# Optimization experiments

Hardware: AMD Instinct MI355X
Metric: run time of the kernel (lower is better)

Reference implementation:

```python
import jax, jax.numpy as jnp
import numpy as np

EPS = 1e-08
SURROGATE_SCALE = 10.0  # SuperSpike surrogate slope

@jax.custom_vjp
def spike_fn(v):
    # Heaviside forward, SuperSpike surrogate gradient backward
    return (v > 0).astype(v.dtype)

def _spike_fwd(v):
    return spike_fn(v), v

def _spike_bwd(v, g):
    return (g / (1.0 + SURROGATE_SCALE * jnp.abs(v)) ** 2,)

spike_fn.defvjp(_spike_fwd, _spike_bwd)


def setup_inputs() -> dict:
    key = jax.random.key(0)
    k1, k2, k3, k4 = jax.random.split(key, 4)
    B, C, T = 64, 256, 2048
    x = jax.random.normal(k1, (B, C, T), dtype=jnp.float32)
    conv_weight = jax.random.normal(k2, (C, C, 3), dtype=jnp.float32) * 0.05
    beta = jnp.clip(0.7 + 0.01 * jax.random.normal(k3, (1,), dtype=jnp.float32), 0.0, 1.0)
    b = jnp.clip(1.0 + 0.01 * jax.random.normal(k4, (C,), dtype=jnp.float32), 0.0, None)
    return {"x": x, "conv_weight": conv_weight, "beta": beta, "b": b}


def reference(x, conv_weight, beta, b):
    # x: (B, C, T); LIF recurrence over T with scaled threshold/reset
    norm = (conv_weight ** 2).sum((1, 2))          # (C,)
    inv_norm = 1.0 / (norm + EPS)                   # (C,)
    B, C, T = x.shape
    xt = jnp.transpose(x, (2, 0, 1))                # (T, B, C)

    def step(carry, inp):
        mem, spk = carry
        rst = spk * (b * norm)                      # einsum ab,b,b->ab
        mem = (mem - rst) * beta + inp * (1.0 - beta)
        mthr = mem * inv_norm - b
        spk = spike_fn(mthr)
        return (mem, spk), spk

    init = (jnp.zeros((B, C), x.dtype), jnp.zeros((B, C), x.dtype))
    _, spk_rec = jax.lax.scan(step, init, xt)       # (T, B, C)
    return jnp.transpose(spk_rec, (1, 2, 0))        # (B, C, T), flatten_output=False
```

## Files before the change

kernel.cpp:

```cpp
#include <hip/hip_runtime.h>

#define C_DIM 256
#define T_DIM 2048
#define B_DIM 64
#define NROWS (B_DIM * C_DIM)
#define SEGS 8
#define SEGL (T_DIM / SEGS)
#define WARM 128
#define PW   64
#define NPH  ((WARM + SEGL) / PW)
#define WARM_PH (WARM / PW)
#define SPITCH 68
#define NSTR 64

__device__ __forceinline__ float sqrn(float v) { return __fmul_rn(v, v); }

__global__ __launch_bounds__(64) void norm_kernel(const float* __restrict__ w,
                                                  const float* __restrict__ b,
                                                  float* __restrict__ bn,
                                                  float* __restrict__ ninv) {
    const int c = blockIdx.x;
    const int k = threadIdx.x;
    __shared__ float q[8];
    if (k < 8) {
        const float* a = w + c * 768 + k * 96;
        float r0 = sqrn(a[0]), r1 = sqrn(a[1]), r2 = sqrn(a[2]), r3 = sqrn(a[3]);
        float r4 = sqrn(a[4]), r5 = sqrn(a[5]), r6 = sqrn(a[6]), r7 = sqrn(a[7]);
        #pragma unroll
        for (int i = 8; i < 96; i += 8) {
            r0 = __fadd_rn(r0, sqrn(a[i + 0]));
            r1 = __fadd_rn(r1, sqrn(a[i + 1]));
            r2 = __fadd_rn(r2, sqrn(a[i + 2]));
            r3 = __fadd_rn(r3, sqrn(a[i + 3]));
            r4 = __fadd_rn(r4, sqrn(a[i + 4]));
            r5 = __fadd_rn(r5, sqrn(a[i + 5]));
            r6 = __fadd_rn(r6, sqrn(a[i + 6]));
            r7 = __fadd_rn(r7, sqrn(a[i + 7]));
        }
        q[k] = __fadd_rn(__fadd_rn(__fadd_rn(r0, r1), __fadd_rn(r2, r3)),
                         __fadd_rn(__fadd_rn(r4, r5), __fadd_rn(r6, r7)));
    }
    __syncthreads();
    if (k == 0) {
        float s = __fadd_rn(__fadd_rn(__fadd_rn(q[0], q[1]), __fadd_rn(q[2], q[3])),
                            __fadd_rn(__fadd_rn(q[4], q[5]), __fadd_rn(q[6], q[7])));
        bn[c]   = __fmul_rn(b[c], s);
        ninv[c] = 1.0f / __fadd_rn(s, 1e-8f);
    }
}

__device__ __forceinline__ float step_fast(float xw, float& mem, int& mask,
                                           float bnc, float beta, float nic, float bc) {
    float m0 = __fmul_rn(mem, beta);
    float m1 = __fmul_rn(__fsub_rn(mem, bnc), beta);
    m0 = __fadd_rn(m0, xw);
    m1 = __fadd_rn(m1, xw);
    int mi = (__float_as_int(m1) & mask) | (__float_as_int(m0) & ~mask);
    mem = __int_as_float(mi);
    float p = __fmul_rn(mem, nic);
    float d = __fsub_rn(bc, p);
    mask = __float_as_int(d) >> 31;
    return __int_as_float(mask & 0x3f800000);
}

#define STEP4_NOSTORE(v)                                                   \
    do {                                                                   \
        float xw0 = __fmul_rn((v).x, omb);                                 \
        float xw1 = __fmul_rn((v).y, omb);                                 \
        float xw2 = __fmul_rn((v).z, omb);                                 \
        float xw3 = __fmul_rn((v).w, omb);                                 \
        (void)step_fast(xw0, mem, mask, bnc, beta, nic, bc);               \
        (void)step_fast(xw1, mem, mask, bnc, beta, nic, bc);               \
        (void)step_fast(xw2, mem, mask, bnc, beta, nic, bc);               \
        (void)step_fast(xw3, mem, mask, bnc, beta, nic, bc);               \
    } while (0)

#define STEP4_STORE(v, o)                                                  \
    do {                                                                   \
        float xw0 = __fmul_rn((v).x, omb);                                 \
        float xw1 = __fmul_rn((v).y, omb);                                 \
        float xw2 = __fmul_rn((v).z, omb);                                 \
        float xw3 = __fmul_rn((v).w, omb);                                 \
        (o).x = step_fast(xw0, mem, mask, bnc, beta, nic, bc);             \
        (o).y = step_fast(xw1, mem, mask, bnc, beta, nic, bc);             \
        (o).z = step_fast(xw2, mem, mask, bnc, beta, nic, bc);             \
        (o).w = step_fast(xw3, mem, mask, bnc, beta, nic, bc);             \
    } while (0)

#define WAITCNT_LGKM0  0xC07F

__global__ __launch_bounds__(64) void lif_seg_kernel(const float* __restrict__ x,
                                                     const float* __restrict__ beta_p,
                                                     const float* __restrict__ b,
                                                     const float* __restrict__ bn,
                                                     const float* __restrict__ ninv,
                                                     float* __restrict__ out) {
    __shared__ __align__(16) float lds[NSTR * SPITCH];

    const int lane = threadIdx.x;
    const int seg  = lane & 7;
    const int row  = blockIdx.x * 8 + (lane >> 3);
    const int c    = row & (C_DIM - 1);

    const float beta = beta_p[0];
    const float omb  = __fsub_rn(1.0f, beta);
    const float bnc  = bn[c];
    const float nic  = ninv[c];
    const float bc   = b[c];

    const int fh = lane >> 4;
    const int fj = lane & 15;

    float mem = 0.0f;
    int   mask = 0;

    float* my = &lds[lane * SPITCH];

    #pragma unroll 1
    for (int P = 0; P < NPH; ++P) {
        #pragma unroll
        for (int q = 0; q < 16; ++q) {
            const int s    = 4 * q + fh;
            const int srow = blockIdx.x * 8 + (s >> 3);
            int rel = (s & 7) * SEGL - WARM + P * PW;
            if (rel < 0) rel = 0;
            const float* g = x + (size_t)srow * T_DIM + rel + 4 * fj;
            float4 v = *(const float4*)g;
            *(float4*)(&lds[s * SPITCH + 4 * fj]) = v;
        }
        __builtin_amdgcn_s_waitcnt(WAITCNT_LGKM0);

        if (P < WARM_PH) {
            #pragma unroll
            for (int g = 0; g < PW / 4; ++g) {
                float4 v = *(const float4*)(my + 4 * g);
                STEP4_NOSTORE(v);
            }
            if (P == WARM_PH - 1) {
                if (seg == 0) { mem = 0.0f; mask = 0; }
            }
        } else {
            #pragma unroll
            for (int g = 0; g < PW / 4; ++g) {
                float4 v = *(const float4*)(my + 4 * g);
                float4 o;
                STEP4_STORE(v, o);
                *(float4*)(my + 4 * g) = o;
            }
            __builtin_amdgcn_s_waitcnt(WAITCNT_LGKM0);

            #pragma unroll
            for (int q = 0; q < 16; ++q) {
                const int s    = 4 * q + fh;
                const int srow = blockIdx.x * 8 + (s >> 3);
                const int rel  = (s & 7) * SEGL - WARM + P * PW;
                float4 v = *(const float4*)(&lds[s * SPITCH + 4 * fj]);
                *(float4*)(out + (size_t)srow * T_DIM + rel + 4 * fj) = v;
            }
        }
    }
}

extern "C" void kernel_launch(void* const* d_in, const int* in_sizes, int n_in,
                              void* d_out, int out_size, void* d_ws, size_t ws_size,
                              hipStream_t stream) {
    const float* x    = (const float*)d_in[0];
    const float* w    = (const float*)d_in[1];
    const float* beta = (const float*)d_in[2];
    const float* b    = (const float*)d_in[3];
    float* out  = (float*)d_out;
    float* bn   = (float*)d_ws;
    float* ninv = bn + C_DIM;

    norm_kernel<<<C_DIM, 64, 0, stream>>>(w, b, bn, ninv);
    lif_seg_kernel<<<(NROWS * SEGS) / NSTR, NSTR, 0, stream>>>(x, beta, b, bn, ninv, out);
}
```

Baseline: 252.5 us.

## Register-prefetch next phase's input tiles to overlap global loads with compute

```diff
diff --git a/kernel.cpp b/kernel.cpp
--- a/kernel.cpp
+++ b/kernel.cpp
@@ -89,12 +89,18 @@
 
 #define WAITCNT_LGKM0  0xC07F
 
-__global__ __launch_bounds__(64) void lif_seg_kernel(const float* __restrict__ x,
-                                                     const float* __restrict__ beta_p,
-                                                     const float* __restrict__ b,
-                                                     const float* __restrict__ bn,
-                                                     const float* __restrict__ ninv,
-                                                     float* __restrict__ out) {
+#define PF_LIST(M) \
+    M(0, pf0)  M(1, pf1)  M(2, pf2)  M(3, pf3)  \
+    M(4, pf4)  M(5, pf5)  M(6, pf6)  M(7, pf7)  \
+    M(8, pf8)  M(9, pf9)  M(10, pf10) M(11, pf11) \
+    M(12, pf12) M(13, pf13) M(14, pf14) M(15, pf15)
+
+__global__ __launch_bounds__(64, 2) void lif_seg_kernel(const float* __restrict__ x,
+                                                        const float* __restrict__ beta_p,
+                                                        const float* __restrict__ b,
+                                                        const float* __restrict__ bn,
+                                                        const float* __restrict__ ninv,
+                                                        float* __restrict__ out) {
     __shared__ __align__(16) float lds[NSTR * SPITCH];
 
     const int lane = threadIdx.x;
@@ -116,18 +122,43 @@
 
     float* my = &lds[lane * SPITCH];
 
+    float4 pf0, pf1, pf2, pf3, pf4, pf5, pf6, pf7;
+    float4 pf8, pf9, pf10, pf11, pf12, pf13, pf14, pf15;
+
+#define PF_LOAD0(q, v)                                                        \
+    {                                                                         \
+        const int s_    = 4 * (q) + fh;                                       \
+        const int srow_ = blockIdx.x * 8 + (s_ >> 3);                         \
+        int rel_ = (s_ & 7) * SEGL - WARM;                         \
+        if (rel_ < 0) rel_ = 0;         \
+        v = *(const float4*)(x + (size_t)srow_ * T_DIM + rel_ + 4 * fj);      \
+    }
+    PF_LIST(PF_LOAD0)
+#undef PF_LOAD0
+
     #pragma unroll 1
     for (int P = 0; P < NPH; ++P) {
-        #pragma unroll
-        for (int q = 0; q < 16; ++q) {
-            const int s    = 4 * q + fh;
-            const int srow = blockIdx.x * 8 + (s >> 3);
-            int rel = (s & 7) * SEGL - WARM + P * PW;
-            if (rel < 0) rel = 0;
-            const float* g = x + (size_t)srow * T_DIM + rel + 4 * fj;
-            float4 v = *(const float4*)g;
-            *(float4*)(&lds[s * SPITCH + 4 * fj]) = v;
-        }
+#define PF_COMMIT(q, v)                                                       \
+        {                                                                     \
+            const int s_ = 4 * (q) + fh;                                      \
+            *(float4*)(&lds[s_ * SPITCH + 4 * fj]) = v;                       \
+        }
+        PF_LIST(PF_COMMIT)
+#undef PF_COMMIT
+
+        if (P + 1 < NPH) {
+#define PF_LOADN(q, v)                                                        \
+            {                                                                 \
+                const int s_    = 4 * (q) + fh;                               \
+                const int srow_ = blockIdx.x * 8 + (s_ >> 3);                 \
+                int rel_ = (s_ & 7) * SEGL - WARM + (P + 1) * PW;             \
+                if (rel_ < 0) rel_ = 0;           \
+                v = *(const float4*)(x + (size_t)srow_ * T_DIM + rel_ + 4 * fj); \
+            }
+            PF_LIST(PF_LOADN)
+#undef PF_LOADN
+        }
+        __builtin_amdgcn_sched_barrier(0);
         __builtin_amdgcn_s_waitcnt(WAITCNT_LGKM0);
 
         if (P < WARM_PH) {
```

Result: no change. 250.0 us (-1.0%).

## Double-buffer input via direct global-to-LDS loads with XOR swizzle

Applied to the files above, without the earlier changes.

```diff
diff --git a/kernel.cpp b/kernel.cpp
--- a/kernel.cpp
+++ b/kernel.cpp
@@ -7,11 +7,11 @@
 #define SEGS 8
 #define SEGL (T_DIM / SEGS)
 #define WARM 128
-#define PW   64
+#define PW   32
 #define NPH  ((WARM + SEGL) / PW)
 #define WARM_PH (WARM / PW)
-#define SPITCH 68
 #define NSTR 64
+#define BUF_F (NSTR * PW)
 
 __device__ __forceinline__ float sqrn(float v) { return __fmul_rn(v, v); }
 
@@ -88,19 +88,34 @@
     } while (0)
 
 #define WAITCNT_LGKM0  0xC07F
-
-__global__ __launch_bounds__(64) void lif_seg_kernel(const float* __restrict__ x,
-                                                     const float* __restrict__ beta_p,
-                                                     const float* __restrict__ b,
-                                                     const float* __restrict__ bn,
-                                                     const float* __restrict__ ninv,
-                                                     float* __restrict__ out) {
-    __shared__ __align__(16) float lds[NSTR * SPITCH];
+#define WAITVM8()  asm volatile("s_waitcnt vmcnt(8)" ::: "memory")
+#define WAITVM16() asm volatile("s_waitcnt vmcnt(16)" ::: "memory")
+
+__device__ __forceinline__ void dma16(const float* gp, float* lp) {
+    __builtin_amdgcn_global_load_lds(
+        (const __attribute__((address_space(1))) void*)gp,
+        (__attribute__((address_space(3))) void*)lp,
+        16, 0, 0);
+}
+
+__global__ __launch_bounds__(64)
+void lif_seg_kernel(const float* __restrict__ x,
+                    const float* __restrict__ beta_p,
+                    const float* __restrict__ b,
+                    const float* __restrict__ bn,
+                    const float* __restrict__ ninv,
+                    float* __restrict__ out) {
+    __shared__ __align__(16) float lds[2 * BUF_F];
 
     const int lane = threadIdx.x;
     const int seg  = lane & 7;
     const int row  = blockIdx.x * 8 + (lane >> 3);
     const int c    = row & (C_DIM - 1);
+    const int lk   = lane & 7;
+
+    const int ds  = lane >> 3;
+    const int du  = lane & 7;
+    const int swz = du ^ ds;
 
     const float beta = beta_p[0];
     const float omb  = __fsub_rn(1.0f, beta);
@@ -108,32 +123,45 @@
     const float nic  = ninv[c];
     const float bc   = b[c];
 
-    const int fh = lane >> 4;
-    const int fj = lane & 15;
-
     float mem = 0.0f;
     int   mask = 0;
 
-    float* my = &lds[lane * SPITCH];
+    {
+        int rel = ds * SEGL - WARM;
+        if (rel < 0) rel = 0;
+        const float* g = x + rel + 4 * swz;
+        #pragma unroll
+        for (int q = 0; q < 8; ++q) {
+            const size_t grow = (size_t)(blockIdx.x * 8 + q);
+            dma16(g + grow * T_DIM, lds + q * (8 * PW));
+        }
+    }
 
     #pragma unroll 1
     for (int P = 0; P < NPH; ++P) {
-        #pragma unroll
-        for (int q = 0; q < 16; ++q) {
-            const int s    = 4 * q + fh;
-            const int srow = blockIdx.x * 8 + (s >> 3);
-            int rel = (s & 7) * SEGL - WARM + P * PW;
+        const int cur = P & 1;
+        float* buf = lds + cur * BUF_F;
+
+        if (P + 1 < NPH) {
+            int rel = ds * SEGL - WARM + (P + 1) * PW;
             if (rel < 0) rel = 0;
-            const float* g = x + (size_t)srow * T_DIM + rel + 4 * fj;
-            float4 v = *(const float4*)g;
-            *(float4*)(&lds[s * SPITCH + 4 * fj]) = v;
-        }
-        __builtin_amdgcn_s_waitcnt(WAITCNT_LGKM0);
+            const float* g = x + rel + 4 * swz;
+            float* dst = lds + (cur ^ 1) * BUF_F;
+            #pragma unroll
+            for (int q = 0; q < 8; ++q) {
+                const size_t grow = (size_t)(blockIdx.x * 8 + q);
+                dma16(g + grow * T_DIM, dst + q * (8 * PW));
+            }
+        }
+
+        if (P <= WARM_PH || P == NPH - 1) { WAITVM8(); } else { WAITVM16(); }
+
+        float* my = buf + lane * PW;
 
         if (P < WARM_PH) {
             #pragma unroll
             for (int g = 0; g < PW / 4; ++g) {
-                float4 v = *(const float4*)(my + 4 * g);
+                float4 v = *(const float4*)(my + 4 * (g ^ lk));
                 STEP4_NOSTORE(v);
             }
             if (P == WARM_PH - 1) {
@@ -142,20 +170,19 @@
         } else {
             #pragma unroll
             for (int g = 0; g < PW / 4; ++g) {
-                float4 v = *(const float4*)(my + 4 * g);
+                float4 v = *(const float4*)(my + 4 * (g ^ lk));
                 float4 o;
                 STEP4_STORE(v, o);
-                *(float4*)(my + 4 * g) = o;
+                *(float4*)(my + 4 * (g ^ lk)) = o;
             }
             __builtin_amdgcn_s_waitcnt(WAITCNT_LGKM0);
 
-            #pragma unroll
-            for (int q = 0; q < 16; ++q) {
-                const int s    = 4 * q + fh;
-                const int srow = blockIdx.x * 8 + (s >> 3);
-                const int rel  = (s & 7) * SEGL - WARM + P * PW;
-                float4 v = *(const float4*)(&lds[s * SPITCH + 4 * fj]);
-                *(float4*)(out + (size_t)srow * T_DIM + rel + 4 * fj) = v;
+            const int rel = ds * SEGL - WARM + P * PW;
+            #pragma unroll
+            for (int q = 0; q < 8; ++q) {
+                const size_t grow = (size_t)(blockIdx.x * 8 + q);
+                float4 v = *(const float4*)(buf + (8 * q + ds) * PW + 4 * swz);
+                *(float4*)(out + grow * T_DIM + rel + 4 * du) = v;
             }
         }
     }
```

Result: no change. 255.3 us (+1.1%).

## Stage whole rows into LDS via global_load_lds with 16 segments per row

Applied to the files above, without the earlier changes.

```diff
diff --git a/kernel.cpp b/kernel.cpp
--- a/kernel.cpp
+++ b/kernel.cpp
@@ -4,14 +4,12 @@
 #define T_DIM 2048
 #define B_DIM 64
 #define NROWS (B_DIM * C_DIM)
-#define SEGS 8
+#define RPB  4
+#define SEGS 16
 #define SEGL (T_DIM / SEGS)
 #define WARM 128
-#define PW   64
-#define NPH  ((WARM + SEGL) / PW)
-#define WARM_PH (WARM / PW)
-#define SPITCH 68
-#define NSTR 64
+#define WG   (WARM / 4)
+#define EG   (SEGL / 4)
 
 __device__ __forceinline__ float sqrn(float v) { return __fmul_rn(v, v); }
 
@@ -89,18 +87,27 @@
 
 #define WAITCNT_LGKM0  0xC07F
 
-__global__ __launch_bounds__(64) void lif_seg_kernel(const float* __restrict__ x,
-                                                     const float* __restrict__ beta_p,
-                                                     const float* __restrict__ b,
-                                                     const float* __restrict__ bn,
-                                                     const float* __restrict__ ninv,
-                                                     float* __restrict__ out) {
-    __shared__ __align__(16) float lds[NSTR * SPITCH];
+__device__ __forceinline__ void dma16(const float* gp, float* lp) {
+    __builtin_amdgcn_global_load_lds(
+        (const __attribute__((address_space(1))) void*)gp,
+        (__attribute__((address_space(3))) void*)lp,
+        16, 0, 0);
+}
+
+__global__ __launch_bounds__(64)
+void lif_seg_kernel(const float* __restrict__ x,
+                    const float* __restrict__ beta_p,
+                    const float* __restrict__ b,
+                    const float* __restrict__ bn,
+                    const float* __restrict__ ninv,
+                    float* __restrict__ out) {
+    __shared__ __align__(16) float lds[RPB * T_DIM];
 
     const int lane = threadIdx.x;
-    const int seg  = lane & 7;
-    const int row  = blockIdx.x * 8 + (lane >> 3);
-    const int c    = row & (C_DIM - 1);
+    const int row  = lane >> 4;
+    const int seg  = lane & 15;
+    const size_t grow = (size_t)blockIdx.x * RPB + row;
+    const int c    = (int)(grow & (C_DIM - 1));
 
     const float beta = beta_p[0];
     const float omb  = __fsub_rn(1.0f, beta);
@@ -108,56 +115,57 @@
     const float nic  = ninv[c];
     const float bc   = b[c];
 
-    const int fh = lane >> 4;
-    const int fj = lane & 15;
+    const size_t xbase = (size_t)blockIdx.x * RPB * T_DIM;
 
+    #pragma unroll
+    for (int j = 0; j < 32; ++j) {
+        const int rj = j >> 3, cj = j & 7;
+        const int p  = cj * 64 + lane;
+        const int l  = p ^ ((p >> 5) & 7);
+        dma16(x + xbase + (size_t)rj * T_DIM + 4 * l,
+              lds + rj * T_DIM + cj * 256);
+    }
+    asm volatile("s_waitcnt vmcnt(0)" ::: "memory");
+
+    float* rbase = lds + row * T_DIM;
     float mem = 0.0f;
     int   mask = 0;
 
-    float* my = &lds[lane * SPITCH];
+    {
+        const int wl0  = (seg - 1) * 32;
+        const int wkey = (seg - 1) & 7;
+        const float* wp = rbase + 4 * (wl0 < 0 ? 0 : wl0);
+        const int live = (seg != 0);
+        #pragma unroll 4
+        for (int G = 0; G < WG; ++G) {
+            const int u = live ? (G ^ wkey) : 0;
+            float4 v = *(const float4*)(wp + 4 * u);
+            STEP4_NOSTORE(v);
+        }
+        if (seg == 0) { mem = 0.0f; mask = 0; }
+    }
 
-    #pragma unroll 1
-    for (int P = 0; P < NPH; ++P) {
-        #pragma unroll
-        for (int q = 0; q < 16; ++q) {
-            const int s    = 4 * q + fh;
-            const int srow = blockIdx.x * 8 + (s >> 3);
-            int rel = (s & 7) * SEGL - WARM + P * PW;
-            if (rel < 0) rel = 0;
-            const float* g = x + (size_t)srow * T_DIM + rel + 4 * fj;
-            float4 v = *(const float4*)g;
-            *(float4*)(&lds[s * SPITCH + 4 * fj]) = v;
+    {
+        const int key = seg & 7;
+        float* ep = rbase + 4 * (seg * 32);
+        #pragma unroll 4
+        for (int G = 0; G < EG; ++G) {
+            float* a = ep + 4 * (G ^ key);
+            float4 v = *(const float4*)a;
+            float4 o;
+            STEP4_STORE(v, o);
+            *(float4*)a = o;
         }
-        __builtin_amdgcn_s_waitcnt(WAITCNT_LGKM0);
+    }
+    __builtin_amdgcn_s_waitcnt(WAITCNT_LGKM0);
 
-        if (P < WARM_PH) {
-            #pragma unroll
-            for (int g = 0; g < PW / 4; ++g) {
-                float4 v = *(const float4*)(my + 4 * g);
-                STEP4_NOSTORE(v);
-            }
-            if (P == WARM_PH - 1) {
-                if (seg == 0) { mem = 0.0f; mask = 0; }
-            }
-        } else {
-            #pragma unroll
-            for (int g = 0; g < PW / 4; ++g) {
-                float4 v = *(const float4*)(my + 4 * g);
-                float4 o;
-                STEP4_STORE(v, o);
-                *(float4*)(my + 4 * g) = o;
-            }
-            __builtin_amdgcn_s_waitcnt(WAITCNT_LGKM0);
-
-            #pragma unroll
-            for (int q = 0; q < 16; ++q) {
-                const int s    = 4 * q + fh;
-                const int srow = blockIdx.x * 8 + (s >> 3);
-                const int rel  = (s & 7) * SEGL - WARM + P * PW;
-                float4 v = *(const float4*)(&lds[s * SPITCH + 4 * fj]);
-                *(float4*)(out + (size_t)srow * T_DIM + rel + 4 * fj) = v;
-            }
-        }
+    #pragma unroll
+    for (int j = 0; j < 32; ++j) {
+        const int rj = j >> 3, cj = j & 7;
+        const int p  = cj * 64 + lane;
+        const int l  = p ^ ((p >> 5) & 7);
+        float4 v = *(const float4*)(lds + rj * T_DIM + 4 * p);
+        *(float4*)(out + xbase + (size_t)rj * T_DIM + 4 * l) = v;
     }
 }
 
@@ -173,5 +181,5 @@
     float* ninv = bn + C_DIM;
 
     norm_kernel<<<C_DIM, 64, 0, stream>>>(w, b, bn, ninv);
-    lif_seg_kernel<<<(NROWS * SEGS) / NSTR, NSTR, 0, stream>>>(x, beta, b, bn, ninv, out);
+    lif_seg_kernel<<<NROWS / RPB, 64, 0, stream>>>(x, beta, b, bn, ninv, out);
 }
```

After: 252.2 us. Within noise of the previous version (-0.1%).
